# Optimization experiments

Measured on AMD Instinct MI355X. Metric: run time of the kernel, lower is better.

The kernel has to match this reference:

```python
import jax, jax.numpy as jnp
import numpy as np

# Concrete func with analytic derivatives: f(x,a,b) = sigmoid(a*x + b)
# s' = s(1-s); s'' = s(1-s)(1-2s); s''' = s(1-s)(1-6s+6s^2)

def setup_inputs() -> dict:
    key = jax.random.key(0)
    k1, k2, k3, k4, k5 = jax.random.split(key, 5)
    B, N = 2048, 8192
    return {
        "x": jax.random.normal(k1, (B, N), dtype=jnp.float32),
        "a": jax.random.uniform(k2, (B, 1), dtype=jnp.float32) + 0.5,
        "b": jax.random.normal(k3, (B, 1), dtype=jnp.float32) * 0.1,
        "mean": jax.random.uniform(k4, (B, 1), dtype=jnp.float32),
        "var": jax.random.uniform(k5, (B, 1), dtype=jnp.float32) * 0.1,
        "dim": 1,
    }


def reference(x, a, b, mean, var, dim):
    ax = dim
    m = lambda t: jnp.mean(t, axis=ax, keepdims=True)

    u = a * x + b
    s = jax.nn.sigmoid(u)
    sp = s * (1.0 - s)            # f'
    spp = sp * (1.0 - 2.0 * s)    # f''

    f = s
    df_da = sp * x
    df_db = sp
    d2f_da2 = spp * x * x
    d2f_dab = spp * x
    d2f_db2 = spp

    fm = m(f)
    em = fm - mean
    dem_da = m(df_da)
    dem_db = m(df_db)
    d2em_da2 = m(d2f_da2)
    d2em_dab = m(d2f_dab)
    d2em_db2 = m(d2f_db2)

    ev = m(f * f) - fm ** 2 - var
    dev_da = 2 * (m(f * df_da) - fm * dem_da)
    dev_db = 2 * (m(f * df_db) - fm * dem_db)
    d2ev_da2 = 2 * (m(df_da ** 2 + f * d2f_da2) - dem_da ** 2 - fm * d2em_da2)
    d2ev_dab = 2 * (m(df_da * df_db + f * d2f_dab) - dem_da * dem_db - fm * d2em_dab)
    d2ev_db2 = 2 * (m(df_db ** 2 + f * d2f_db2) - dem_db ** 2 - fm * d2em_db2)

    dl_da = 2 * (em * dem_da + ev * dev_da)
    dl_db = 2 * (em * dem_db + ev * dev_db)
    d2l_da2 = 2 * (dem_da ** 2 + em * d2em_da2 + dev_da ** 2 + ev * d2ev_da2)
    d2l_dab = 2 * (dem_da * dem_db + em * d2em_dab + dev_da * dev_db + ev * d2ev_dab)
    d2l_db2 = 2 * (dem_db ** 2 + em * d2em_db2 + dev_db ** 2 + ev * d2ev_db2)

    den = d2l_da2 * d2l_db2 - d2l_dab ** 2
    na = (dl_da * d2l_db2 - dl_db * d2l_dab) / den
    nb = (dl_db * d2l_da2 - dl_da * d2l_dab) / den
    return (na, nb)
```

## Files before the change

### kernel.cpp

```cpp
#include <hip/hip_runtime.h>
#include <cmath>


#define THREADS 256

__device__ __forceinline__ float fast_exp2(float t) {
#if __has_builtin(__builtin_amdgcn_exp2f)
    return __builtin_amdgcn_exp2f(t);
#else
    return exp2f(t);
#endif
}

__device__ __forceinline__ float fast_rcp(float t) {
#if __has_builtin(__builtin_amdgcn_rcpf)
    return __builtin_amdgcn_rcpf(t);
#else
    return 1.0f / t;
#endif
}

__global__ __launch_bounds__(THREADS) void nsab_kernel(
    const float* __restrict__ x,
    const float* __restrict__ a,
    const float* __restrict__ b,
    const float* __restrict__ meanp,
    const float* __restrict__ varp,
    float* __restrict__ out,
    int B, int N)
{
    const int row = blockIdx.x;
    const int tid = threadIdx.x;

    const float av = a[row];
    const float bv = b[row];
    const float LOG2E = 1.4426950408889634f;
    const float c1 = -av * LOG2E;
    const float c0 = -bv * LOG2E;

    const float4* __restrict__ xr = (const float4*)(x + (size_t)row * (size_t)N);
    const int nvec = N >> 2;

    float A1 = 0.f, A2 = 0.f, A3 = 0.f, A4 = 0.f;
    float B1 = 0.f, B2 = 0.f, B3 = 0.f, B4 = 0.f;
    float C1 = 0.f, C2 = 0.f, C3 = 0.f, C4 = 0.f;

    #define NSAB_PROC(xx_)  do {                                        \
        const float xx = (xx_);                                         \
        const float e  = fast_exp2(fmaf(c1, xx, c0));                   \
        const float s  = fast_rcp(1.0f + e);                            \
        const float s2 = s * s;                                         \
        const float s3 = s2 * s;                                        \
        const float s4 = s2 * s2;                                       \
        const float x2 = xx * xx;                                       \
        A1 += s;  A2 += s2;  A3 += s3;  A4 += s4;                       \
        B1 = fmaf(s,  xx, B1);  B2 = fmaf(s2, xx, B2);                  \
        B3 = fmaf(s3, xx, B3);  B4 = fmaf(s4, xx, B4);                  \
        C1 = fmaf(s,  x2, C1);  C2 = fmaf(s2, x2, C2);                  \
        C3 = fmaf(s3, x2, C3);  C4 = fmaf(s4, x2, C4);                  \
    } while (0)

    #define NSAB_PROC4(v)  do {                                         \
        NSAB_PROC((v).x); NSAB_PROC((v).y);                             \
        NSAB_PROC((v).z); NSAB_PROC((v).w);                             \
    } while (0)

    if (nvec == 8 * THREADS) {
        const float4* p = xr + tid;
        float4 v0 = p[0 * THREADS];
        float4 v1 = p[1 * THREADS];
        float4 v2 = p[2 * THREADS];
        float4 v3 = p[3 * THREADS];
        float4 v4 = p[4 * THREADS];
        float4 v5 = p[5 * THREADS];
        float4 v6 = p[6 * THREADS];
        float4 v7 = p[7 * THREADS];
        NSAB_PROC4(v0); NSAB_PROC4(v1); NSAB_PROC4(v2); NSAB_PROC4(v3);
        NSAB_PROC4(v4); NSAB_PROC4(v5); NSAB_PROC4(v6); NSAB_PROC4(v7);
    } else {
        int i = tid;
        if (i < nvec) {
            float4 cur = xr[i];
            #pragma unroll 1
            for (; i + THREADS < nvec; i += THREADS) {
                float4 nxt = xr[i + THREADS];
                NSAB_PROC4(cur);
                cur = nxt;
            }
            NSAB_PROC4(cur);
        }
    }
    #undef NSAB_PROC4
    #undef NSAB_PROC

    float acc[12] = {A1, A2, A3, A4, B1, B2, B3, B4, C1, C2, C3, C4};

    #pragma unroll
    for (int k = 0; k < 12; ++k) {
        float v = acc[k];
        #pragma unroll
        for (int off = 32; off > 0; off >>= 1)
            v += __shfl_down(v, off, 64);
        acc[k] = v;
    }

    __shared__ float part[THREADS / 64][12];
    const int wave = tid >> 6;
    const int lane = tid & 63;
    if (lane == 0) {
        #pragma unroll
        for (int k = 0; k < 12; ++k) part[wave][k] = acc[k];
    }
    __syncthreads();

    if (tid == 0) {
        double S[12];
        #pragma unroll
        for (int k = 0; k < 12; ++k)
            S[k] = (double)part[0][k] + (double)part[1][k]
                 + (double)part[2][k] + (double)part[3][k];

        const double invN = 1.0 / (double)N;
        const double M1 = S[0] * invN, M2 = S[1] * invN;
        const double M3 = S[2] * invN, M4 = S[3] * invN;
        const double X1 = S[4] * invN, X2 = S[5] * invN;
        const double X3 = S[6] * invN, X4 = S[7] * invN;
        const double Y1 = S[8] * invN, Y2 = S[9] * invN;
        const double Y3 = S[10] * invN, Y4 = S[11] * invN;

        const double fm       = M1;
        const double mff      = M2;
        const double dem_db   = M1 - M2;
        const double dem_da   = X1 - X2;
        const double d2em_db2 = M1 - 3.0 * M2 + 2.0 * M3;
        const double d2em_dab = X1 - 3.0 * X2 + 2.0 * X3;
        const double d2em_da2 = Y1 - 3.0 * Y2 + 2.0 * Y3;
        const double m_fdfb   = M2 - M3;
        const double m_fdfa   = X2 - X3;
        const double m_w      = 2.0 * M2 - 5.0 * M3 + 3.0 * M4;
        const double m_wx     = 2.0 * X2 - 5.0 * X3 + 3.0 * X4;
        const double m_wx2    = 2.0 * Y2 - 5.0 * Y3 + 3.0 * Y4;

        const double mv = (double)meanp[row];
        const double vv = (double)varp[row];

        const double em = fm - mv;
        const double ev = mff - fm * fm - vv;
        const double dev_da = 2.0 * (m_fdfa - fm * dem_da);
        const double dev_db = 2.0 * (m_fdfb - fm * dem_db);
        const double d2ev_da2 = 2.0 * (m_wx2 - dem_da * dem_da - fm * d2em_da2);
        const double d2ev_dab = 2.0 * (m_wx  - dem_da * dem_db - fm * d2em_dab);
        const double d2ev_db2 = 2.0 * (m_w   - dem_db * dem_db - fm * d2em_db2);

        const double dl_da = 2.0 * (em * dem_da + ev * dev_da);
        const double dl_db = 2.0 * (em * dem_db + ev * dev_db);
        const double d2l_da2 = 2.0 * (dem_da * dem_da + em * d2em_da2
                                    + dev_da * dev_da + ev * d2ev_da2);
        const double d2l_dab = 2.0 * (dem_da * dem_db + em * d2em_dab
                                    + dev_da * dev_db + ev * d2ev_dab);
        const double d2l_db2 = 2.0 * (dem_db * dem_db + em * d2em_db2
                                    + dev_db * dev_db + ev * d2ev_db2);

        const double den = d2l_da2 * d2l_db2 - d2l_dab * d2l_dab;
        const double na = (dl_da * d2l_db2 - dl_db * d2l_dab) / den;
        const double nb = (dl_db * d2l_da2 - dl_da * d2l_dab) / den;

        out[row]     = (float)na;
        out[B + row] = (float)nb;
    }
}

extern "C" void kernel_launch(void* const* d_in, const int* in_sizes, int n_in,
                              void* d_out, int out_size, void* d_ws, size_t ws_size,
                              hipStream_t stream) {
    const float* x    = (const float*)d_in[0];
    const float* a    = (const float*)d_in[1];
    const float* b    = (const float*)d_in[2];
    const float* mean = (const float*)d_in[3];
    const float* var  = (const float*)d_in[4];
    const int B = in_sizes[1];
    const int N = in_sizes[0] / B;
    float* out = (float*)d_out;

    nsab_kernel<<<dim3(B), dim3(THREADS), 0, stream>>>(x, a, b, mean, var, out, B, N);
}
```

Before: 100.7 us.

## Assign one wavefront per row with prefetched loop, dropping block-level reduction

Result: no change. 100.7 us (-0.0%).

```diff
diff --git a/kernel.cpp b/kernel.cpp
--- a/kernel.cpp
+++ b/kernel.cpp
@@ -20,7 +20,140 @@
 #endif
 }
 
-__global__ __launch_bounds__(THREADS) void nsab_kernel(
+__device__ __forceinline__ void nsab_epilogue(
+    const double* S, int N, double mv, double vv,
+    float* __restrict__ out, int B, int row)
+{
+    const double invN = 1.0 / (double)N;
+    const double M1 = S[0] * invN, M2 = S[1] * invN;
+    const double M3 = S[2] * invN, M4 = S[3] * invN;
+    const double X1 = S[4] * invN, X2 = S[5] * invN;
+    const double X3 = S[6] * invN, X4 = S[7] * invN;
+    const double Y1 = S[8] * invN, Y2 = S[9] * invN;
+    const double Y3 = S[10] * invN, Y4 = S[11] * invN;
+
+    const double fm       = M1;
+    const double mff      = M2;
+    const double dem_db   = M1 - M2;
+    const double dem_da   = X1 - X2;
+    const double d2em_db2 = M1 - 3.0 * M2 + 2.0 * M3;
+    const double d2em_dab = X1 - 3.0 * X2 + 2.0 * X3;
+    const double d2em_da2 = Y1 - 3.0 * Y2 + 2.0 * Y3;
+    const double m_fdfb   = M2 - M3;
+    const double m_fdfa   = X2 - X3;
+    const double m_w      = 2.0 * M2 - 5.0 * M3 + 3.0 * M4;
+    const double m_wx     = 2.0 * X2 - 5.0 * X3 + 3.0 * X4;
+    const double m_wx2    = 2.0 * Y2 - 5.0 * Y3 + 3.0 * Y4;
+
+    const double em = fm - mv;
+    const double ev = mff - fm * fm - vv;
+    const double dev_da = 2.0 * (m_fdfa - fm * dem_da);
+    const double dev_db = 2.0 * (m_fdfb - fm * dem_db);
+    const double d2ev_da2 = 2.0 * (m_wx2 - dem_da * dem_da - fm * d2em_da2);
+    const double d2ev_dab = 2.0 * (m_wx  - dem_da * dem_db - fm * d2em_dab);
+    const double d2ev_db2 = 2.0 * (m_w   - dem_db * dem_db - fm * d2em_db2);
+
+    const double dl_da = 2.0 * (em * dem_da + ev * dev_da);
+    const double dl_db = 2.0 * (em * dem_db + ev * dev_db);
+    const double d2l_da2 = 2.0 * (dem_da * dem_da + em * d2em_da2
+                                + dev_da * dev_da + ev * d2ev_da2);
+    const double d2l_dab = 2.0 * (dem_da * dem_db + em * d2em_dab
+                                + dev_da * dev_db + ev * d2ev_dab);
+    const double d2l_db2 = 2.0 * (dem_db * dem_db + em * d2em_db2
+                                + dev_db * dev_db + ev * d2ev_db2);
+
+    const double den = d2l_da2 * d2l_db2 - d2l_dab * d2l_dab;
+    const double na = (dl_da * d2l_db2 - dl_db * d2l_dab) / den;
+    const double nb = (dl_db * d2l_da2 - dl_da * d2l_dab) / den;
+
+    out[row]     = (float)na;
+    out[B + row] = (float)nb;
+}
+
+#define NSAB_PROC(xx_)  do {                                        \
+    const float xx = (xx_);                                         \
+    const float e  = fast_exp2(fmaf(c1, xx, c0));                   \
+    const float s  = fast_rcp(1.0f + e);                            \
+    const float s2 = s * s;                                         \
+    const float s3 = s2 * s;                                        \
+    const float s4 = s2 * s2;                                       \
+    const float x2 = xx * xx;                                       \
+    A1 += s;  A2 += s2;  A3 += s3;  A4 += s4;                       \
+    B1 = fmaf(s,  xx, B1);  B2 = fmaf(s2, xx, B2);                  \
+    B3 = fmaf(s3, xx, B3);  B4 = fmaf(s4, xx, B4);                  \
+    C1 = fmaf(s,  x2, C1);  C2 = fmaf(s2, x2, C2);                  \
+    C3 = fmaf(s3, x2, C3);  C4 = fmaf(s4, x2, C4);                  \
+} while (0)
+
+#define NSAB_PROC4(v)  do {                                         \
+    NSAB_PROC((v).x); NSAB_PROC((v).y);                             \
+    NSAB_PROC((v).z); NSAB_PROC((v).w);                             \
+} while (0)
+
+__global__ __launch_bounds__(THREADS) void nsab_kernel_wpr(
+    const float* __restrict__ x,
+    const float* __restrict__ a,
+    const float* __restrict__ b,
+    const float* __restrict__ meanp,
+    const float* __restrict__ varp,
+    float* __restrict__ out,
+    int B, int N)
+{
+    const int wave = threadIdx.x >> 6;
+    const int lane = threadIdx.x & 63;
+    const int row  = (blockIdx.x << 2) | wave;
+
+    const float av = a[row];
+    const float bv = b[row];
+    const float LOG2E = 1.4426950408889634f;
+    const float c1 = -av * LOG2E;
+    const float c0 = -bv * LOG2E;
+
+    const float4* __restrict__ p =
+        (const float4*)(x + (size_t)row * (size_t)N) + lane;
+
+    float A1 = 0.f, A2 = 0.f, A3 = 0.f, A4 = 0.f;
+    float B1 = 0.f, B2 = 0.f, B3 = 0.f, B4 = 0.f;
+    float C1 = 0.f, C2 = 0.f, C3 = 0.f, C4 = 0.f;
+
+    float4 v0 = p[0 * 64], v1 = p[1 * 64], v2 = p[2 * 64], v3 = p[3 * 64],
+           v4 = p[4 * 64], v5 = p[5 * 64], v6 = p[6 * 64], v7 = p[7 * 64];
+
+    #pragma unroll 1
+    for (int g = 1; g < 4; ++g) {
+        const float4* __restrict__ q = p + (size_t)g * 512;
+        NSAB_PROC4(v0); v0 = q[0 * 64];
+        NSAB_PROC4(v1); v1 = q[1 * 64];
+        NSAB_PROC4(v2); v2 = q[2 * 64];
+        NSAB_PROC4(v3); v3 = q[3 * 64];
+        NSAB_PROC4(v4); v4 = q[4 * 64];
+        NSAB_PROC4(v5); v5 = q[5 * 64];
+        NSAB_PROC4(v6); v6 = q[6 * 64];
+        NSAB_PROC4(v7); v7 = q[7 * 64];
+    }
+    NSAB_PROC4(v0); NSAB_PROC4(v1); NSAB_PROC4(v2); NSAB_PROC4(v3);
+    NSAB_PROC4(v4); NSAB_PROC4(v5); NSAB_PROC4(v6); NSAB_PROC4(v7);
+
+    float acc[12] = {A1, A2, A3, A4, B1, B2, B3, B4, C1, C2, C3, C4};
+
+    #pragma unroll
+    for (int k = 0; k < 12; ++k) {
+        float v = acc[k];
+        #pragma unroll
+        for (int off = 32; off > 0; off >>= 1)
+            v += __shfl_down(v, off, 64);
+        acc[k] = v;
+    }
+
+    if (lane == 0) {
+        double S[12];
+        #pragma unroll
+        for (int k = 0; k < 12; ++k) S[k] = (double)acc[k];
+        nsab_epilogue(S, N, (double)meanp[row], (double)varp[row], out, B, row);
+    }
+}
+
+__global__ __launch_bounds__(THREADS) void nsab_kernel_generic(
     const float* __restrict__ x,
     const float* __restrict__ a,
     const float* __restrict__ b,
@@ -45,53 +178,17 @@
     float B1 = 0.f, B2 = 0.f, B3 = 0.f, B4 = 0.f;
     float C1 = 0.f, C2 = 0.f, C3 = 0.f, C4 = 0.f;
 
-    #define NSAB_PROC(xx_)  do {                                        \
-        const float xx = (xx_);                                         \
-        const float e  = fast_exp2(fmaf(c1, xx, c0));                   \
-        const float s  = fast_rcp(1.0f + e);                            \
-        const float s2 = s * s;                                         \
-        const float s3 = s2 * s;                                        \
-        const float s4 = s2 * s2;                                       \
-        const float x2 = xx * xx;                                       \
-        A1 += s;  A2 += s2;  A3 += s3;  A4 += s4;                       \
-        B1 = fmaf(s,  xx, B1);  B2 = fmaf(s2, xx, B2);                  \
-        B3 = fmaf(s3, xx, B3);  B4 = fmaf(s4, xx, B4);                  \
-        C1 = fmaf(s,  x2, C1);  C2 = fmaf(s2, x2, C2);                  \
-        C3 = fmaf(s3, x2, C3);  C4 = fmaf(s4, x2, C4);                  \
-    } while (0)
-
-    #define NSAB_PROC4(v)  do {                                         \
-        NSAB_PROC((v).x); NSAB_PROC((v).y);                             \
-        NSAB_PROC((v).z); NSAB_PROC((v).w);                             \
-    } while (0)
-
-    if (nvec == 8 * THREADS) {
-        const float4* p = xr + tid;
-        float4 v0 = p[0 * THREADS];
-        float4 v1 = p[1 * THREADS];
-        float4 v2 = p[2 * THREADS];
-        float4 v3 = p[3 * THREADS];
-        float4 v4 = p[4 * THREADS];
-        float4 v5 = p[5 * THREADS];
-        float4 v6 = p[6 * THREADS];
-        float4 v7 = p[7 * THREADS];
-        NSAB_PROC4(v0); NSAB_PROC4(v1); NSAB_PROC4(v2); NSAB_PROC4(v3);
-        NSAB_PROC4(v4); NSAB_PROC4(v5); NSAB_PROC4(v6); NSAB_PROC4(v7);
-    } else {
-        int i = tid;
-        if (i < nvec) {
-            float4 cur = xr[i];
-            #pragma unroll 1
-            for (; i + THREADS < nvec; i += THREADS) {
-                float4 nxt = xr[i + THREADS];
-                NSAB_PROC4(cur);
-                cur = nxt;
-            }
+    int i = tid;
+    if (i < nvec) {
+        float4 cur = xr[i];
+        #pragma unroll 1
+        for (; i + THREADS < nvec; i += THREADS) {
+            float4 nxt = xr[i + THREADS];
             NSAB_PROC4(cur);
+            cur = nxt;
         }
-    }
-    #undef NSAB_PROC4
-    #undef NSAB_PROC
+        NSAB_PROC4(cur);
+    }
 
     float acc[12] = {A1, A2, A3, A4, B1, B2, B3, B4, C1, C2, C3, C4};
 
@@ -119,54 +216,7 @@
         for (int k = 0; k < 12; ++k)
             S[k] = (double)part[0][k] + (double)part[1][k]
                  + (double)part[2][k] + (double)part[3][k];
-
-        const double invN = 1.0 / (double)N;
-        const double M1 = S[0] * invN, M2 = S[1] * invN;
-        const double M3 = S[2] * invN, M4 = S[3] * invN;
-        const double X1 = S[4] * invN, X2 = S[5] * invN;
-        const double X3 = S[6] * invN, X4 = S[7] * invN;
-        const double Y1 = S[8] * invN, Y2 = S[9] * invN;
-        const double Y3 = S[10] * invN, Y4 = S[11] * invN;
-
-        const double fm       = M1;
-        const double mff      = M2;
-        const double dem_db   = M1 - M2;
-        const double dem_da   = X1 - X2;
-        const double d2em_db2 = M1 - 3.0 * M2 + 2.0 * M3;
-        const double d2em_dab = X1 - 3.0 * X2 + 2.0 * X3;
-        const double d2em_da2 = Y1 - 3.0 * Y2 + 2.0 * Y3;
-        const double m_fdfb   = M2 - M3;
-        const double m_fdfa   = X2 - X3;
-        const double m_w      = 2.0 * M2 - 5.0 * M3 + 3.0 * M4;
-        const double m_wx     = 2.0 * X2 - 5.0 * X3 + 3.0 * X4;
-        const double m_wx2    = 2.0 * Y2 - 5.0 * Y3 + 3.0 * Y4;
-
-        const double mv = (double)meanp[row];
-        const double vv = (double)varp[row];
-
-        const double em = fm - mv;
-        const double ev = mff - fm * fm - vv;
-        const double dev_da = 2.0 * (m_fdfa - fm * dem_da);
-        const double dev_db = 2.0 * (m_fdfb - fm * dem_db);
-        const double d2ev_da2 = 2.0 * (m_wx2 - dem_da * dem_da - fm * d2em_da2);
-        const double d2ev_dab = 2.0 * (m_wx  - dem_da * dem_db - fm * d2em_dab);
-        const double d2ev_db2 = 2.0 * (m_w   - dem_db * dem_db - fm * d2em_db2);
-
-        const double dl_da = 2.0 * (em * dem_da + ev * dev_da);
-        const double dl_db = 2.0 * (em * dem_db + ev * dev_db);
-        const double d2l_da2 = 2.0 * (dem_da * dem_da + em * d2em_da2
-                                    + dev_da * dev_da + ev * d2ev_da2);
-        const double d2l_dab = 2.0 * (dem_da * dem_db + em * d2em_dab
-                                    + dev_da * dev_db + ev * d2ev_dab);
-        const double d2l_db2 = 2.0 * (dem_db * dem_db + em * d2em_db2
-                                    + dev_db * dev_db + ev * d2ev_db2);
-
-        const double den = d2l_da2 * d2l_db2 - d2l_dab * d2l_dab;
-        const double na = (dl_da * d2l_db2 - dl_db * d2l_dab) / den;
-        const double nb = (dl_db * d2l_da2 - dl_da * d2l_dab) / den;
-
-        out[row]     = (float)na;
-        out[B + row] = (float)nb;
+        nsab_epilogue(S, N, (double)meanp[row], (double)varp[row], out, B, row);
     }
 }
 
@@ -182,5 +232,11 @@
     const int N = in_sizes[0] / B;
     float* out = (float*)d_out;
 
-    nsab_kernel<<<dim3(B), dim3(THREADS), 0, stream>>>(x, a, b, mean, var, out, B, N);
-}
+    if (N == 8192 && (B & 3) == 0) {
+        nsab_kernel_wpr<<<dim3(B >> 2), dim3(THREADS), 0, stream>>>(
+            x, a, b, mean, var, out, B, N);
+    } else {
+        nsab_kernel_generic<<<dim3(B), dim3(THREADS), 0, stream>>>(
+            x, a, b, mean, var, out, B, N);
+    }
+}
```
